# Optimization experiments

Hardware: AMD Instinct MI355X
Metric: run time of the kernel (lower is better)

The kernel has to match this reference:

```python
import jax, jax.numpy as jnp
import numpy as np

NUM_HEADS = 12

def setup_inputs() -> dict:
    key = jax.random.key(0)
    k1, k2, k3 = jax.random.split(key, 3)
    B, N, D = 16, 1024, 768
    x = jax.random.normal(k1, (B, N, D), dtype=jnp.float32)
    w_qkv = jax.random.normal(k2, (D, 3 * D), dtype=jnp.float32) * (D ** -0.5)
    b_qkv = jnp.zeros((3 * D,), dtype=jnp.float32)
    w_proj = jax.random.normal(k3, (D, D), dtype=jnp.float32) * (D ** -0.5)
    b_proj = jnp.zeros((D,), dtype=jnp.float32)
    return {"x": x, "w_qkv": w_qkv, "b_qkv": b_qkv, "w_proj": w_proj, "b_proj": b_proj}

def reference(x, w_qkv, b_qkv, w_proj, b_proj):
    B, N, D = x.shape
    H = NUM_HEADS
    Hd = D // H
    scale = Hd ** -0.5
    qkv = x @ w_qkv + b_qkv                       # (B, N, 3D)
    qkv = qkv.reshape(B, N, 3, H, Hd)
    q, k, v = qkv[:, :, 0], qkv[:, :, 1], qkv[:, :, 2]  # (B, N, H, Hd)
    attn = jnp.einsum('bnhd,bmhd->bhnm', q, k) * scale  # (B, H, N, N)
    attn = jax.nn.softmax(attn, axis=-1)
    out = jnp.einsum('bhnm,bmhd->bnhd', attn, v).reshape(B, N, D)
    return out @ w_proj + b_proj
```

## Files before the change

kernel.cpp:

```cpp
#include <hip/hip_runtime.h>


typedef _Float16 half8 __attribute__((ext_vector_type(8)));
typedef _Float16 half4 __attribute__((ext_vector_type(4)));
typedef __fp16   fp16x2 __attribute__((ext_vector_type(2)));
typedef float    f32x4  __attribute__((ext_vector_type(4)));
typedef float    f32x16 __attribute__((ext_vector_type(16)));
typedef unsigned int u32x4 __attribute__((ext_vector_type(4)));

#define DI __device__ __forceinline__

constexpr int   BATCH  = 16;
constexpr int   SEQ    = 1024;
constexpr int   DM     = 768;
constexpr int   NH     = 12;
constexpr int   HD     = 64;
constexpr float SCALE  = 0.125f;
constexpr float LOG2E  = 1.4426950408889634f;

DI void copy16(_Float16* dst, const _Float16* src) {
  *(u32x4*)dst = *(const u32x4*)src;
}

DI int pack_rtz(float a, float b) {
  union { fp16x2 h; int i; } u;
  u.h = __builtin_amdgcn_cvt_pkrtz(a, b);
  return u.i;
}

__global__ void cvt_x_kernel(const float* __restrict__ x,
                             _Float16* __restrict__ xh, int n4) {
  int i = blockIdx.x * 256 + threadIdx.x;
  if (i >= n4) return;
  float4 v = ((const float4*)x)[i];
  half4 h;
  h[0] = (_Float16)v.x; h[1] = (_Float16)v.y;
  h[2] = (_Float16)v.z; h[3] = (_Float16)v.w;
  *(half4*)(xh + (size_t)i * 4) = h;
}

__global__ void cvt_wt2_kernel(const float* __restrict__ wq,
                               _Float16* __restrict__ wqT,
                               const float* __restrict__ wp,
                               _Float16* __restrict__ wpT) {
  __shared__ float tile[32][33];
  const int by = blockIdx.y;
  const float* w; _Float16* wt; int N, nb;
  if (by < 72) { w = wq; wt = wqT; N = 2304; nb = by * 32; }
  else         { w = wp; wt = wpT; N = 768;  nb = (by - 72) * 32; }
  const int K = 768;
  int kb = blockIdx.x * 32;
  int tx = threadIdx.x & 31, ty = threadIdx.x >> 5;
#pragma unroll
  for (int i = 0; i < 32; i += 8)
    tile[ty + i][tx] = w[(size_t)(kb + ty + i) * N + nb + tx];
  __syncthreads();
#pragma unroll
  for (int i = 0; i < 32; i += 8)
    wt[(size_t)(nb + ty + i) * K + kb + tx] = (_Float16)tile[tx][ty + i];
}

__launch_bounds__(256, 3)
__global__ void gemm_qkv_kernel(const _Float16* __restrict__ A,
                                const _Float16* __restrict__ Bt,
                                const float* __restrict__ bias,
                                _Float16* __restrict__ Qo,
                                _Float16* __restrict__ Ko,
                                _Float16* __restrict__ VTo) {
  __shared__ _Float16 sh[20480];
  _Float16* Cs = sh;
  const int tid  = threadIdx.x;
  const int lin  = blockIdx.x;
  const int xcd  = lin & 7, j = lin >> 3;
  const int ct   = j % 18;
  const int m0   = ((j / 18) * 8 + xcd) * 128;
  const int n0   = ct * 128;
  const int w    = tid >> 6, lane = tid & 63;
  const int quad = lane >> 4, l15 = lane & 15;
  const int wr   = w >> 1, wc = w & 1;

  f32x4 acc[4][4] = {};

  const int e  = tid * 8;
  const int rA = e >> 5;
  const int g8 = e & 31;
  const _Float16* ga = A  + (size_t)(m0 + rA) * 768 + g8;
  const _Float16* gb = Bt + (size_t)(n0 + rA) * 768 + g8;
  const int so = rA * 40 + g8;

  u32x4 pA0 = *(const u32x4*)ga;
  u32x4 pA1 = *(const u32x4*)(ga + 64 * 768);
  u32x4 pB0 = *(const u32x4*)gb;
  u32x4 pB1 = *(const u32x4*)(gb + 64 * 768);
  {
    _Float16* As = sh; _Float16* Bs = sh + 5120;
    *(u32x4*)(As + so) = pA0; *(u32x4*)(As + so + 64 * 40) = pA1;
    *(u32x4*)(Bs + so) = pB0; *(u32x4*)(Bs + so + 64 * 40) = pB1;
  }

  for (int kt = 0; kt < 24; ++kt) {
    __syncthreads();
    if (kt < 23) {
      const int k0 = (kt + 1) * 32;
      pA0 = *(const u32x4*)(ga + k0);
      pA1 = *(const u32x4*)(ga + k0 + 64 * 768);
      pB0 = *(const u32x4*)(gb + k0);
      pB1 = *(const u32x4*)(gb + k0 + 64 * 768);
    }
    const _Float16* As = sh + (kt & 1) * 10240;
    const _Float16* Bs = As + 5120;

    half8 af[4], bf[4];
#pragma unroll
    for (int mi = 0; mi < 4; mi++)
      af[mi] = *(const half8*)&As[(wr * 64 + mi * 16 + l15) * 40 + quad * 8];
#pragma unroll
    for (int ni = 0; ni < 4; ni++)
      bf[ni] = *(const half8*)&Bs[(wc * 64 + ni * 16 + l15) * 40 + quad * 8];
#pragma unroll
    for (int mi = 0; mi < 4; mi++)
#pragma unroll
      for (int ni = 0; ni < 4; ni++)
        acc[mi][ni] = __builtin_amdgcn_mfma_f32_16x16x32_f16(
            af[mi], bf[ni], acc[mi][ni], 0, 0, 0);

    if (kt < 23) {
      _Float16* Asn = sh + ((kt + 1) & 1) * 10240;
      _Float16* Bsn = Asn + 5120;
      *(u32x4*)(Asn + so) = pA0; *(u32x4*)(Asn + so + 64 * 40) = pA1;
      *(u32x4*)(Bsn + so) = pB0; *(u32x4*)(Bsn + so + 64 * 40) = pB1;
    }
  }
  __syncthreads();

  const float oscale = (ct < 6) ? SCALE : 1.0f;
  float bcol[4];
#pragma unroll
  for (int ni = 0; ni < 4; ni++)
    bcol[ni] = bias[n0 + wc * 64 + ni * 16 + l15];

  const int b     = m0 >> 10;
  const int nrow0 = m0 & 1023;
  const int sec   = ct / 6;
  const int h0    = (ct % 6) * 2;

#pragma unroll
  for (int p = 0; p < 2; ++p) {
    if (p) __syncthreads();
    if (wr == p) {
#pragma unroll
      for (int mi = 0; mi < 4; mi++)
#pragma unroll
        for (int ni = 0; ni < 4; ni++) {
          int col = wc * 64 + ni * 16 + l15;
          int row = mi * 16 + quad * 4;
#pragma unroll
          for (int r = 0; r < 4; r++)
            Cs[(row + r) * 136 + col] =
                (_Float16)((acc[mi][ni][r] + bcol[ni]) * oscale);
        }
    }
    __syncthreads();

    if (sec < 2) {
      _Float16* dst = (sec == 0) ? Qo : Ko;
      int row = tid >> 2, seg = tid & 3;
      int hl = seg >> 1, off32 = (seg & 1) * 32;
      _Float16* g = dst +
          ((size_t)((b * NH + h0 + hl) * SEQ + nrow0 + p * 64 + row)) * HD + off32;
      const _Float16* s = &Cs[row * 136 + hl * 64 + off32];
      copy16(g, s);
      copy16(g + 8, s + 8);
      copy16(g + 16, s + 16);
      copy16(g + 24, s + 24);
    } else {
      int c = tid & 127, half = tid >> 7;
      int hl = c >> 6, d = c & 63;
      _Float16 tmp[32];
#pragma unroll
      for (int jj = 0; jj < 32; jj++) tmp[jj] = Cs[(half * 32 + jj) * 136 + c];
      _Float16* g = VTo + ((size_t)((b * NH + h0 + hl) * HD + d)) * SEQ
                        + nrow0 + p * 64 + half * 32;
#pragma unroll
      for (int jj = 0; jj < 4; jj++)
        copy16(g + jj * 8, (const _Float16*)&tmp[jj * 8]);
    }
  }
}

__launch_bounds__(256, 2)
__global__ void attn_kernel(const _Float16* __restrict__ Q,
                            const _Float16* __restrict__ K,
                            const _Float16* __restrict__ VT,
                            _Float16* __restrict__ Oh) {
  __shared__ _Float16 smem[2][2][64 * 72];
  _Float16* OLds = &smem[0][0][0];

  const int tid = threadIdx.x;
  const int i   = blockIdx.x;
  const int bh  = (i & 7) * 24 + ((i >> 3) >> 2);
  const int q0  = ((i >> 3) & 3) * 256;
  const int b   = bh / NH, hh = bh - b * NH;
  const int w   = tid >> 6, lane = tid & 63;
  const int l31 = lane & 31, h = lane >> 5;

  const _Float16* Qg = Q  + (size_t)bh * SEQ * HD;
  const _Float16* Kg = K  + (size_t)bh * SEQ * HD;
  const _Float16* Vg = VT + (size_t)bh * HD * SEQ;

  half8 qb[2][4];
#pragma unroll
  for (int N = 0; N < 2; N++) {
    const _Float16* qrow = Qg + (size_t)(q0 + w * 64 + N * 32 + l31) * HD + h * 8;
#pragma unroll
    for (int s = 0; s < 4; s++)
      qb[N][s] = *(const half8*)(qrow + s * 16);
  }

  const int  sr  = (tid & 127) >> 1;
  const int  sp  = tid & 1;
  const bool isK = tid < 128;
  const _Float16* sg = isK ? (Kg + sr * HD + sp * 32)
                           : (Vg + (size_t)sr * SEQ + sp * 32);
  const int sstep = isK ? 64 * HD : 64;
  const int soff  = (isK ? 0 : 64 * 72) + sr * 72 + sp * 32;

  u32x4 pf[4];
#pragma unroll
  for (int c = 0; c < 4; c++) pf[c] = *(const u32x4*)(sg + c * 8);
#pragma unroll
  for (int c = 0; c < 4; c++) *(u32x4*)(&smem[0][0][0] + soff + c * 8) = pf[c];

  f32x16 of[2][2];
#pragma unroll
  for (int D = 0; D < 2; D++)
#pragma unroll
    for (int N = 0; N < 2; N++)
#pragma unroll
      for (int r = 0; r < 16; r++) of[D][N][r] = 0.f;
  float m_[2] = {-1e30f, -1e30f}, l_[2] = {0.f, 0.f};

  for (int kt = 0; kt < 16; ++kt) {
    if (kt < 15) {
      const _Float16* nsg = sg + (kt + 1) * sstep;
#pragma unroll
      for (int c = 0; c < 4; c++) pf[c] = *(const u32x4*)(nsg + c * 8);
    }
    __syncthreads();
    const _Float16* Ks = &smem[kt & 1][0][0];
    const _Float16* Vs = &smem[kt & 1][1][0];

    f32x16 sf[2][2];
#pragma unroll
    for (int M = 0; M < 2; M++)
#pragma unroll
      for (int N = 0; N < 2; N++)
#pragma unroll
        for (int r = 0; r < 16; r++) sf[M][N][r] = 0.f;
#pragma unroll
    for (int s = 0; s < 4; s++) {
      half8 ka0 = *(const half8*)&Ks[l31 * 72 + s * 16 + h * 8];
      half8 ka1 = *(const half8*)&Ks[(32 + l31) * 72 + s * 16 + h * 8];
#pragma unroll
      for (int N = 0; N < 2; N++) {
        sf[0][N] = __builtin_amdgcn_mfma_f32_32x32x16_f16(ka0, qb[N][s], sf[0][N], 0, 0, 0);
        sf[1][N] = __builtin_amdgcn_mfma_f32_32x32x16_f16(ka1, qb[N][s], sf[1][N], 0, 0, 0);
      }
    }

    float alpha[2], c1[2], tsum[2];
#pragma unroll
    for (int N = 0; N < 2; N++) {
      float tmax = -1e30f;
#pragma unroll
      for (int r = 0; r < 16; r++)
        tmax = fmaxf(tmax, fmaxf(sf[0][N][r], sf[1][N][r]));
      tmax = fmaxf(tmax, __shfl_xor(tmax, 32, 64));
      float mnew = fmaxf(m_[N], tmax);
      alpha[N] = __builtin_amdgcn_exp2f((m_[N] - mnew) * LOG2E);
      m_[N] = mnew;
      c1[N] = mnew * LOG2E;
      tsum[N] = 0.f;
    }

    int pdw[2][2][8];
#pragma unroll
    for (int M = 0; M < 2; M++)
#pragma unroll
      for (int N = 0; N < 2; N++) {
#pragma unroll
        for (int r = 0; r < 16; r++) {
          float p = __builtin_amdgcn_exp2f(sf[M][N][r] * LOG2E - c1[N]);
          sf[M][N][r] = p;
          tsum[N] += p;
        }
#pragma unroll
        for (int u = 0; u < 8; u++)
          pdw[M][N][u] = pack_rtz(sf[M][N][2 * u], sf[M][N][2 * u + 1]);
      }
#pragma unroll
    for (int N = 0; N < 2; N++) {
      tsum[N] += __shfl_xor(tsum[N], 32, 64);
      l_[N] = l_[N] * alpha[N] + tsum[N];
    }
#pragma unroll
    for (int D = 0; D < 2; D++)
#pragma unroll
      for (int N = 0; N < 2; N++)
#pragma unroll
        for (int r = 0; r < 16; r++) of[D][N][r] *= alpha[N];

#pragma unroll
    for (int t = 0; t < 4; ++t) {
      const int M = t >> 1, s2 = (t & 1) * 4;
      half8 va0 = *(const half8*)&Vs[l31 * 72 + t * 16 + h * 8];
      half8 va1 = *(const half8*)&Vs[(32 + l31) * 72 + t * 16 + h * 8];
#pragma unroll
      for (int N = 0; N < 2; N++) {
        int a0 = pdw[M][N][s2 + 0], a1 = pdw[M][N][s2 + 1];
        int a2 = pdw[M][N][s2 + 2], a3 = pdw[M][N][s2 + 3];
        int e0 = h ? a0 : a2, e1 = h ? a1 : a3;
        int r0 = __shfl_xor(e0, 32, 64), r1 = __shfl_xor(e1, 32, 64);
        union { u32x4 u; half8 hv; } bb;
        bb.u[0] = h ? r0 : a0; bb.u[1] = h ? r1 : a1;
        bb.u[2] = h ? a2 : r0; bb.u[3] = h ? a3 : r1;
        of[0][N] = __builtin_amdgcn_mfma_f32_32x32x16_f16(va0, bb.hv, of[0][N], 0, 0, 0);
        of[1][N] = __builtin_amdgcn_mfma_f32_32x32x16_f16(va1, bb.hv, of[1][N], 0, 0, 0);
      }
    }

    if (kt < 15) {
      _Float16* dst = &smem[(kt + 1) & 1][0][0] + soff;
#pragma unroll
      for (int c = 0; c < 4; c++) *(u32x4*)(dst + c * 8) = pf[c];
    }
  }

  __syncthreads();
  float inv[2] = {1.0f / l_[0], 1.0f / l_[1]};
  int* OW = (int*)OLds;
#pragma unroll
  for (int N = 0; N < 2; N++) {
    const int q_local = w * 64 + N * 32 + l31;
#pragma unroll
    for (int D = 0; D < 2; D++)
#pragma unroll
      for (int u = 0; u < 8; u++) {
        int v = pack_rtz(of[D][N][2 * u] * inv[N], of[D][N][2 * u + 1] * inv[N]);
        int dwi = 16 * D + 4 * (u >> 1) + (u & 1) + 2 * h;
        OW[q_local * 36 + dwi] = v;
      }
  }
  __syncthreads();
#pragma unroll
  for (int p = 0; p < 8; p++) {
    int q = p * 32 + (tid >> 3), c = tid & 7;
    *(u32x4*)(Oh + (size_t)(b * SEQ + q0 + q) * DM + hh * HD + c * 8) =
        *(const u32x4*)&OLds[q * 72 + c * 8];
  }
}

__launch_bounds__(256, 3)
__global__ void gemm_proj_kernel(const _Float16* __restrict__ A,
                                 const _Float16* __restrict__ Bt,
                                 const float* __restrict__ bias,
                                 float* __restrict__ out) {
  __shared__ _Float16 sh[20480];
  const int tid  = threadIdx.x;
  const int lin  = blockIdx.x;
  const int xcd  = lin & 7, j = lin >> 3;
  const int ct   = j % 6;
  const int m0   = ((j / 6) * 8 + xcd) * 128;
  const int n0   = ct * 128;
  const int w    = tid >> 6, lane = tid & 63;
  const int quad = lane >> 4, l15 = lane & 15;
  const int wr   = w >> 1, wc = w & 1;

  f32x4 acc[4][4] = {};

  const int e  = tid * 8;
  const int rA = e >> 5;
  const int g8 = e & 31;
  const _Float16* ga = A  + (size_t)(m0 + rA) * 768 + g8;
  const _Float16* gb = Bt + (size_t)(n0 + rA) * 768 + g8;
  const int so = rA * 40 + g8;

  u32x4 pA0 = *(const u32x4*)ga;
  u32x4 pA1 = *(const u32x4*)(ga + 64 * 768);
  u32x4 pB0 = *(const u32x4*)gb;
  u32x4 pB1 = *(const u32x4*)(gb + 64 * 768);
  {
    _Float16* As = sh; _Float16* Bs = sh + 5120;
    *(u32x4*)(As + so) = pA0; *(u32x4*)(As + so + 64 * 40) = pA1;
    *(u32x4*)(Bs + so) = pB0; *(u32x4*)(Bs + so + 64 * 40) = pB1;
  }

  for (int kt = 0; kt < 24; ++kt) {
    __syncthreads();
    if (kt < 23) {
      const int k0 = (kt + 1) * 32;
      pA0 = *(const u32x4*)(ga + k0);
      pA1 = *(const u32x4*)(ga + k0 + 64 * 768);
      pB0 = *(const u32x4*)(gb + k0);
      pB1 = *(const u32x4*)(gb + k0 + 64 * 768);
    }
    const _Float16* As = sh + (kt & 1) * 10240;
    const _Float16* Bs = As + 5120;

    half8 af[4], bf[4];
#pragma unroll
    for (int mi = 0; mi < 4; mi++)
      af[mi] = *(const half8*)&As[(wr * 64 + mi * 16 + l15) * 40 + quad * 8];
#pragma unroll
    for (int ni = 0; ni < 4; ni++)
      bf[ni] = *(const half8*)&Bs[(wc * 64 + ni * 16 + l15) * 40 + quad * 8];
#pragma unroll
    for (int mi = 0; mi < 4; mi++)
#pragma unroll
      for (int ni = 0; ni < 4; ni++)
        acc[mi][ni] = __builtin_amdgcn_mfma_f32_16x16x32_f16(
            af[mi], bf[ni], acc[mi][ni], 0, 0, 0);

    if (kt < 23) {
      _Float16* Asn = sh + ((kt + 1) & 1) * 10240;
      _Float16* Bsn = Asn + 5120;
      *(u32x4*)(Asn + so) = pA0; *(u32x4*)(Asn + so + 64 * 40) = pA1;
      *(u32x4*)(Bsn + so) = pB0; *(u32x4*)(Bsn + so + 64 * 40) = pB1;
    }
  }

  float bcol[4];
#pragma unroll
  for (int ni = 0; ni < 4; ni++)
    bcol[ni] = bias[n0 + wc * 64 + ni * 16 + l15];
#pragma unroll
  for (int mi = 0; mi < 4; mi++)
#pragma unroll
    for (int ni = 0; ni < 4; ni++) {
      int col = n0 + wc * 64 + ni * 16 + l15;
      int row = m0 + wr * 64 + mi * 16 + quad * 4;
#pragma unroll
      for (int r = 0; r < 4; r++)
        out[(size_t)(row + r) * 768 + col] = acc[mi][ni][r] + bcol[ni];
    }
}

extern "C" void kernel_launch(void* const* d_in, const int* in_sizes, int n_in,
                              void* d_out, int out_size, void* d_ws, size_t ws_size,
                              hipStream_t stream) {
  const float* x      = (const float*)d_in[0];
  const float* w_qkv  = (const float*)d_in[1];
  const float* b_qkv  = (const float*)d_in[2];
  const float* w_proj = (const float*)d_in[3];
  const float* b_proj = (const float*)d_in[4];
  float* out = (float*)d_out;

  char* ws = (char*)d_ws;
  _Float16* xh     = (_Float16*)(ws);
  _Float16* wqkvT  = (_Float16*)(ws + 25165824);
  _Float16* wprojT = (_Float16*)(ws + 28704768);
  _Float16* Qp     = (_Float16*)(ws + 29884416);
  _Float16* Kp     = (_Float16*)(ws + 55050240);
  _Float16* VTp    = (_Float16*)(ws + 80216064);
  _Float16* Ohp    = (_Float16*)(ws + 105381888);

  cvt_x_kernel<<<dim3(3145728 / 256), 256, 0, stream>>>(x, xh, 3145728);
  cvt_wt2_kernel<<<dim3(24, 96), 256, 0, stream>>>(w_qkv, wqkvT, w_proj, wprojT);
  gemm_qkv_kernel<<<dim3(2304), 256, 0, stream>>>(xh, wqkvT, b_qkv, Qp, Kp, VTp);
  attn_kernel<<<dim3(768), 256, 0, stream>>>(Qp, Kp, VTp, Ohp);
  gemm_proj_kernel<<<dim3(768), 256, 0, stream>>>(Ohp, wprojT, b_proj, out);
}
```

Baseline: 309.1 us.

## Stage GEMM tiles with direct global-to-LDS async loads instead of register staging

Both the QKV and projection GEMMs now fill their double-buffered LDS tiles with the global_load_lds builtin, writing 16 bytes per lane straight into shared memory. This replaces the old path of loading into registers and storing to LDS after the MFMA block. Each wave's lanes are remapped so that the hardware's lane-contiguous LDS writes land in the right tile rows. Dropping the register round-trip frees VGPRs and instructions, and lets the next tile's fetch overlap the current tile's math. The cost is losing the 40-element row padding: rows now use a stride of 32, so fragment reads may hit more LDS bank conflicts. LDS use drops from 40KB to 32KB per block.

```diff
diff --git a/kernel.cpp b/kernel.cpp
--- a/kernel.cpp
+++ b/kernel.cpp
@@ -26,6 +26,12 @@
   union { fp16x2 h; int i; } u;
   u.h = __builtin_amdgcn_cvt_pkrtz(a, b);
   return u.i;
+}
+
+DI void gld16(const _Float16* g, _Float16* l) {
+  __builtin_amdgcn_global_load_lds(
+      (const __attribute__((address_space(1))) void*)g,
+      (__attribute__((address_space(3))) void*)l, 16, 0, 0);
 }
 
 __global__ void cvt_x_kernel(const float* __restrict__ x,
@@ -67,7 +73,7 @@
                                 _Float16* __restrict__ Qo,
                                 _Float16* __restrict__ Ko,
                                 _Float16* __restrict__ VTo) {
-  __shared__ _Float16 sh[20480];
+  __shared__ _Float16 sh[16384];
   _Float16* Cs = sh;
   const int tid  = threadIdx.x;
   const int lin  = blockIdx.x;
@@ -81,55 +87,45 @@
 
   f32x4 acc[4][4] = {};
 
-  const int e  = tid * 8;
-  const int rA = e >> 5;
-  const int g8 = e & 31;
-  const _Float16* ga = A  + (size_t)(m0 + rA) * 768 + g8;
-  const _Float16* gb = Bt + (size_t)(n0 + rA) * 768 + g8;
-  const int so = rA * 40 + g8;
-
-  u32x4 pA0 = *(const u32x4*)ga;
-  u32x4 pA1 = *(const u32x4*)(ga + 64 * 768);
-  u32x4 pB0 = *(const u32x4*)gb;
-  u32x4 pB1 = *(const u32x4*)(gb + 64 * 768);
-  {
-    _Float16* As = sh; _Float16* Bs = sh + 5120;
-    *(u32x4*)(As + so) = pA0; *(u32x4*)(As + so + 64 * 40) = pA1;
-    *(u32x4*)(Bs + so) = pB0; *(u32x4*)(Bs + so + 64 * 40) = pB1;
-  }
+  const int g0 = tid + w * 64;
+  const int r0 = g0 >> 2, s0 = g0 & 3;
+  const _Float16* gaA = A  + (size_t)(m0 + r0) * 768 + s0 * 8;
+  const _Float16* gaB = Bt + (size_t)(n0 + r0) * 768 + s0 * 8;
+  const int ldst = w * 1024;
+
+  auto STAGE = [&](int buf, int kt) {
+    _Float16* As = sh + buf * 8192;
+    _Float16* Bs = As + 4096;
+    const _Float16* a = gaA + kt * 32;
+    const _Float16* b = gaB + kt * 32;
+    gld16(a,            As + ldst);
+    gld16(a + 16 * 768, As + ldst + 512);
+    gld16(b,            Bs + ldst);
+    gld16(b + 16 * 768, Bs + ldst + 512);
+  };
+
+  STAGE(0, 0);
 
   for (int kt = 0; kt < 24; ++kt) {
     __syncthreads();
-    if (kt < 23) {
-      const int k0 = (kt + 1) * 32;
-      pA0 = *(const u32x4*)(ga + k0);
-      pA1 = *(const u32x4*)(ga + k0 + 64 * 768);
-      pB0 = *(const u32x4*)(gb + k0);
-      pB1 = *(const u32x4*)(gb + k0 + 64 * 768);
-    }
-    const _Float16* As = sh + (kt & 1) * 10240;
-    const _Float16* Bs = As + 5120;
+    if (kt < 23) STAGE((kt + 1) & 1, kt + 1);
+
+    const _Float16* As = sh + (kt & 1) * 8192;
+    const _Float16* Bs = As + 4096;
 
     half8 af[4], bf[4];
 #pragma unroll
     for (int mi = 0; mi < 4; mi++)
-      af[mi] = *(const half8*)&As[(wr * 64 + mi * 16 + l15) * 40 + quad * 8];
+      af[mi] = *(const half8*)&As[(wr * 64 + mi * 16 + l15) * 32 + quad * 8];
 #pragma unroll
     for (int ni = 0; ni < 4; ni++)
-      bf[ni] = *(const half8*)&Bs[(wc * 64 + ni * 16 + l15) * 40 + quad * 8];
+      bf[ni] = *(const half8*)&Bs[(wc * 64 + ni * 16 + l15) * 32 + quad * 8];
 #pragma unroll
     for (int mi = 0; mi < 4; mi++)
 #pragma unroll
       for (int ni = 0; ni < 4; ni++)
         acc[mi][ni] = __builtin_amdgcn_mfma_f32_16x16x32_f16(
             af[mi], bf[ni], acc[mi][ni], 0, 0, 0);
-
-    if (kt < 23) {
-      _Float16* Asn = sh + ((kt + 1) & 1) * 10240;
-      _Float16* Bsn = Asn + 5120;
-      *(u32x4*)(Asn + so) = pA0; *(u32x4*)(Asn + so + 64 * 40) = pA1;
-      *(u32x4*)(Bsn + so) = pB0; *(u32x4*)(Bsn + so + 64 * 40) = pB1;
-    }
   }
   __syncthreads();
 
@@ -365,7 +361,7 @@
                                  const _Float16* __restrict__ Bt,
                                  const float* __restrict__ bias,
                                  float* __restrict__ out) {
-  __shared__ _Float16 sh[20480];
+  __shared__ _Float16 sh[16384];
   const int tid  = threadIdx.x;
   const int lin  = blockIdx.x;
   const int xcd  = lin & 7, j = lin >> 3;
@@ -378,55 +374,45 @@
 
   f32x4 acc[4][4] = {};
 
-  const int e  = tid * 8;
-  const int rA = e >> 5;
-  const int g8 = e & 31;
-  const _Float16* ga = A  + (size_t)(m0 + rA) * 768 + g8;
-  const _Float16* gb = Bt + (size_t)(n0 + rA) * 768 + g8;
-  const int so = rA * 40 + g8;
-
-  u32x4 pA0 = *(const u32x4*)ga;
-  u32x4 pA1 = *(const u32x4*)(ga + 64 * 768);
-  u32x4 pB0 = *(const u32x4*)gb;
-  u32x4 pB1 = *(const u32x4*)(gb + 64 * 768);
-  {
-    _Float16* As = sh; _Float16* Bs = sh + 5120;
-    *(u32x4*)(As + so) = pA0; *(u32x4*)(As + so + 64 * 40) = pA1;
-    *(u32x4*)(Bs + so) = pB0; *(u32x4*)(Bs + so + 64 * 40) = pB1;
-  }
+  const int g0 = tid + w * 64;
+  const int r0 = g0 >> 2, s0 = g0 & 3;
+  const _Float16* gaA = A  + (size_t)(m0 + r0) * 768 + s0 * 8;
+  const _Float16* gaB = Bt + (size_t)(n0 + r0) * 768 + s0 * 8;
+  const int ldst = w * 1024;
+
+  auto STAGE = [&](int buf, int kt) {
+    _Float16* As = sh + buf * 8192;
+    _Float16* Bs = As + 4096;
+    const _Float16* a = gaA + kt * 32;
+    const _Float16* b = gaB + kt * 32;
+    gld16(a,            As + ldst);
+    gld16(a + 16 * 768, As + ldst + 512);
+    gld16(b,            Bs + ldst);
+    gld16(b + 16 * 768, Bs + ldst + 512);
+  };
+
+  STAGE(0, 0);
 
   for (int kt = 0; kt < 24; ++kt) {
     __syncthreads();
-    if (kt < 23) {
-      const int k0 = (kt + 1) * 32;
-      pA0 = *(const u32x4*)(ga + k0);
-      pA1 = *(const u32x4*)(ga + k0 + 64 * 768);
-      pB0 = *(const u32x4*)(gb + k0);
-      pB1 = *(const u32x4*)(gb + k0 + 64 * 768);
-    }
-    const _Float16* As = sh + (kt & 1) * 10240;
-    const _Float16* Bs = As + 5120;
+    if (kt < 23) STAGE((kt + 1) & 1, kt + 1);
+
+    const _Float16* As = sh + (kt & 1) * 8192;
+    const _Float16* Bs = As + 4096;
 
     half8 af[4], bf[4];
 #pragma unroll
     for (int mi = 0; mi < 4; mi++)
-      af[mi] = *(const half8*)&As[(wr * 64 + mi * 16 + l15) * 40 + quad * 8];
+      af[mi] = *(const half8*)&As[(wr * 64 + mi * 16 + l15) * 32 + quad * 8];
 #pragma unroll
     for (int ni = 0; ni < 4; ni++)
-      bf[ni] = *(const half8*)&Bs[(wc * 64 + ni * 16 + l15) * 40 + quad * 8];
+      bf[ni] = *(const half8*)&Bs[(wc * 64 + ni * 16 + l15) * 32 + quad * 8];
 #pragma unroll
     for (int mi = 0; mi < 4; mi++)
 #pragma unroll
       for (int ni = 0; ni < 4; ni++)
         acc[mi][ni] = __builtin_amdgcn_mfma_f32_16x16x32_f16(
             af[mi], bf[ni], acc[mi][ni], 0, 0, 0);
-
-    if (kt < 23) {
-      _Float16* Asn = sh + ((kt + 1) & 1) * 10240;
-      _Float16* Bsn = Asn + 5120;
-      *(u32x4*)(Asn + so) = pA0; *(u32x4*)(Asn + so + 64 * 40) = pA1;
-      *(u32x4*)(Bsn + so) = pB0; *(u32x4*)(Bsn + so + 64 * 40) = pB1;
-    }
   }
 
   float bcol[4];
```

After: 311.2 us. No clear change (+0.7%).
